# Kernel optimization log

Hardware: AMD Instinct MI355X
Metric: run time of the kernel (lower is better)

Reference implementation:

```python
import jax, jax.numpy as jnp
import numpy as np

# Sizes (match input_specs)
B = 50                 # number of CRN graphs in the batch
NS_PER, NR_PER = 2000, 4000
N_S, N_R = B * NS_PER, B * NR_PER   # 100k species, 200k reactions total
E = 1_000_000          # bipartite edges
D = 128                # d_model
L = 2                  # n_layers
N_TYPES, P_DIM = 16, 8
MAX_SPECIES_IDX = 2000


def setup_inputs() -> dict:
    key = jax.random.key(0)
    ks = jax.random.split(key, 12)
    inp = {
        "species_indices": jax.random.randint(ks[0], (N_S,), 0, MAX_SPECIES_IDX, dtype=jnp.int32),
        "is_external": jax.random.randint(ks[1], (N_S,), 0, 2, dtype=jnp.int32),
        "propensity_type_ids": jax.random.randint(ks[2], (N_R,), 0, N_TYPES, dtype=jnp.int32),
        "propensity_params": jax.random.normal(ks[3], (N_R, P_DIM), dtype=jnp.float32),
        "edge_species": jax.random.randint(ks[4], (E,), 0, N_S, dtype=jnp.int32),
        "edge_reaction": jax.random.randint(ks[5], (E,), 0, N_R, dtype=jnp.int32),
        # contiguous per-graph segment ids (graphs are equal-sized)
        "species_batch": jnp.repeat(jnp.arange(B, dtype=jnp.int32), NS_PER),
        "reaction_batch": jnp.repeat(jnp.arange(B, dtype=jnp.int32), NR_PER),
        # learned parameters
        "species_table": jax.random.normal(ks[6], (MAX_SPECIES_IDX, D), dtype=jnp.float32) * 0.02,
        "external_table": jax.random.normal(ks[7], (2, D), dtype=jnp.float32) * 0.02,
        "type_table": jax.random.normal(ks[8], (N_TYPES, D), dtype=jnp.float32) * 0.02,
        "W_param": jax.random.normal(ks[9], (P_DIM, D), dtype=jnp.float32) * 0.1,
        "b_param": jnp.zeros((D,), dtype=jnp.float32),
        # per-layer message-passing weights: concat([h, msg]) -> d
        "Wr": jax.random.normal(ks[10], (L, 2 * D, D), dtype=jnp.float32) * 0.05,
        "br": jnp.zeros((L, D), dtype=jnp.float32),
        "Ws": jax.random.normal(ks[11], (L, 2 * D, D), dtype=jnp.float32) * 0.05,
        "bs": jnp.zeros((L, D), dtype=jnp.float32),
    }
    return inp


def reference(species_indices, is_external, propensity_type_ids, propensity_params,
              edge_species, edge_reaction, species_batch, reaction_batch,
              species_table, external_table, type_table, W_param, b_param,
              Wr, br, Ws, bs):
    # Initial embeddings
    h_s = species_table[species_indices] + external_table[is_external]          # (N_S, D)
    h_r = type_table[propensity_type_ids] + propensity_params @ W_param + b_param  # (N_R, D)

    n_s, n_r = h_s.shape[0], h_r.shape[0]
    # Alternating bipartite sum message passing (SumMessagePassingLayer)
    for l in range(Wr.shape[0]):
        m_r = jax.ops.segment_sum(h_s[edge_species], edge_reaction, num_segments=n_r)
        h_r = jax.nn.relu(jnp.concatenate([h_r, m_r], axis=-1) @ Wr[l] + br[l])
        m_s = jax.ops.segment_sum(h_r[edge_reaction], edge_species, num_segments=n_s)
        h_s = jax.nn.relu(jnp.concatenate([h_s, m_s], axis=-1) @ Ws[l] + bs[l])

    # Segment-mean pooling per graph (index_add then divide by counts)
    pooled_s = jax.ops.segment_sum(h_s, species_batch, num_segments=B) / float(NS_PER)
    pooled_r = jax.ops.segment_sum(h_r, reaction_batch, num_segments=B) / float(NR_PER)
    context = jnp.concatenate([pooled_s, pooled_r], axis=-1)  # (B, 2D); dropout p=0 -> identity
    return context
```

## Files before the change

### kernel.cpp

```cpp
#include <hip/hip_runtime.h>
#include <stdint.h>

#define NS 100000
#define NR 200000
#define EE 1000000
#define DD 128
#define NB 50
#define NSP 2000
#define NRP 4000
#define BSH 10
#define NBR 196
#define NBS 98
#define CHUNK 8192

typedef short bf16x8 __attribute__((ext_vector_type(8)));
typedef float f32x4 __attribute__((ext_vector_type(4)));
typedef unsigned u32x4 __attribute__((ext_vector_type(4)));
typedef unsigned u32x2 __attribute__((ext_vector_type(2)));

__device__ __forceinline__ unsigned short f2bf(float f){
  unsigned u = __float_as_uint(f);
  u = (u + 0x7FFFu + ((u >> 16) & 1u)) >> 16;
  return (unsigned short)u;
}
__device__ __forceinline__ float bf2f(unsigned short s){
  return __uint_as_float(((unsigned)s) << 16);
}
__device__ __forceinline__ unsigned packbf(float a, float b){
  return (unsigned)f2bf(a) | ((unsigned)f2bf(b) << 16);
}
__device__ __forceinline__ float bflo(unsigned p){ return __uint_as_float(p << 16); }
__device__ __forceinline__ float bfhi(unsigned p){ return __uint_as_float(p & 0xFFFF0000u); }

__global__ void pack_w(const float* __restrict__ Wr, const float* __restrict__ Ws,
                       unsigned short* __restrict__ Wp){
  int g = blockIdx.x*256 + threadIdx.x;
  if (g >= 4*32768) return;
  int j = g & 7; int rest = g >> 3;
  int lane = rest & 63; rest >>= 6;
  int ks = rest & 7; rest >>= 3;
  int ct = rest & 7; int mat = rest >> 3;
  int k  = ks*32 + (lane >> 4)*8 + j;
  int cc = ct*16 + (lane & 15);
  const float* src = (mat < 2) ? (Wr + (size_t)mat*256*DD) : (Ws + (size_t)(mat-2)*256*DD);
  Wp[g] = f2bf(src[(size_t)k*DD + cc]);
}

__global__ __launch_bounds__(256) void init_all(const int* __restrict__ si, const int* __restrict__ ext,
        const int* __restrict__ tid, const float* __restrict__ pp,
        const float* __restrict__ st, const float* __restrict__ et, const float* __restrict__ tt,
        const float* __restrict__ Wpar, const float* __restrict__ bpar,
        unsigned short* __restrict__ hs, unsigned short* __restrict__ hr){
  int g = blockIdx.x*256 + threadIdx.x;
  int row = g >> 4, colb = (g & 15) * 8;
  if (row < NS){
    const float* a = st + (size_t)si[row]*DD + colb;
    const float* b = et + (size_t)ext[row]*DD + colb;
    float4 x0 = ((const float4*)a)[0], x1 = ((const float4*)a)[1];
    float4 y0 = ((const float4*)b)[0], y1 = ((const float4*)b)[1];
    u32x4 o;
    o.x = packbf(x0.x+y0.x, x0.y+y0.y);
    o.y = packbf(x0.z+y0.z, x0.w+y0.w);
    o.z = packbf(x1.x+y1.x, x1.y+y1.y);
    o.w = packbf(x1.z+y1.z, x1.w+y1.w);
    *(u32x4*)(hs + (size_t)row*DD + colb) = o;
  } else {
    int r = row - NS;
    const float* tb = tt + (size_t)tid[r]*DD + colb;
    float4 a0 = ((const float4*)tb)[0], a1 = ((const float4*)tb)[1];
    float4 b0 = ((const float4*)(bpar+colb))[0], b1 = ((const float4*)(bpar+colb))[1];
    a0.x += b0.x; a0.y += b0.y; a0.z += b0.z; a0.w += b0.w;
    a1.x += b1.x; a1.y += b1.y; a1.z += b1.z; a1.w += b1.w;
    const float* pr = pp + (size_t)r*8;
    float4 p0 = ((const float4*)pr)[0], p1 = ((const float4*)pr)[1];
    float w[8] = {p0.x,p0.y,p0.z,p0.w,p1.x,p1.y,p1.z,p1.w};
    #pragma unroll
    for (int p = 0; p < 8; p++){
      float4 w0 = ((const float4*)(Wpar + p*DD + colb))[0];
      float4 w1 = ((const float4*)(Wpar + p*DD + colb))[1];
      a0.x += w[p]*w0.x; a0.y += w[p]*w0.y; a0.z += w[p]*w0.z; a0.w += w[p]*w0.w;
      a1.x += w[p]*w1.x; a1.y += w[p]*w1.y; a1.z += w[p]*w1.z; a1.w += w[p]*w1.w;
    }
    u32x4 o;
    o.x = packbf(a0.x, a0.y); o.y = packbf(a0.z, a0.w);
    o.z = packbf(a1.x, a1.y); o.w = packbf(a1.z, a1.w);
    *(u32x4*)(hr + (size_t)r*DD + colb) = o;
  }
}

__global__ __launch_bounds__(256) void bucket_hist(const int* __restrict__ er, const int* __restrict__ es,
                                                   int* __restrict__ gcnt){
  __shared__ int cnt[NBR + NBS];
  int t = threadIdx.x;
  for (int j = t; j < NBR + NBS; j += 256) cnt[j] = 0;
  __syncthreads();
  long i0 = (long)blockIdx.x * 2048;
  for (int j = t; j < 2048; j += 256){
    long i = i0 + j;
    if (i < EE){
      atomicAdd(&cnt[er[i] >> BSH], 1);
      atomicAdd(&cnt[NBR + (es[i] >> BSH)], 1);
    }
  }
  __syncthreads();
  for (int j = t; j < NBR + NBS; j += 256)
    if (cnt[j]) atomicAdd(&gcnt[j], cnt[j]);
}

__global__ __launch_bounds__(256) void bucket_scan(const int* __restrict__ gcnt,
        int* __restrict__ bktOffR, int* __restrict__ bktOffS,
        int* __restrict__ gCurR, int* __restrict__ gCurS){
  __shared__ int a[256];
  int t = threadIdx.x;
  int own = (t < NBR) ? gcnt[t] : 0;
  a[t] = own; __syncthreads();
  for (int d = 1; d < 256; d <<= 1){
    int x = (t >= d) ? a[t-d] : 0;
    __syncthreads(); a[t] += x; __syncthreads();
  }
  if (t < NBR){ int v = a[t] - own; bktOffR[t] = v; gCurR[t] = v; }
  if (t == 0) bktOffR[NBR] = EE;
  __syncthreads();
  own = (t < NBS) ? gcnt[NBR + t] : 0;
  a[t] = own; __syncthreads();
  for (int d = 1; d < 256; d <<= 1){
    int x = (t >= d) ? a[t-d] : 0;
    __syncthreads(); a[t] += x; __syncthreads();
  }
  if (t < NBS){ int v = a[t] - own; bktOffS[t] = v; gCurS[t] = v; }
  if (t == 0) bktOffS[NBS] = EE;
}

__global__ __launch_bounds__(256) void bin_edges(const int* __restrict__ er, const int* __restrict__ es,
        int* __restrict__ gCurR, int* __restrict__ gCurS,
        unsigned* __restrict__ recR, unsigned* __restrict__ recS){
  __shared__ unsigned stage[CHUNK];
  __shared__ unsigned char stageb[CHUNK];
  __shared__ int cnt[256], scn[256], pref[256], gbase[256], lcur[256];
  int t = threadIdx.x;
  int side = blockIdx.y;
  const int* dest = side ? es : er;
  const int* srca = side ? er : es;
  int* gCur = side ? gCurS : gCurR;
  unsigned* rec = side ? recS : recR;
  int nbkt = side ? NBS : NBR;
  long i0 = (long)blockIdx.x * CHUNK;
  int n = (EE - i0 < CHUNK) ? (int)(EE - i0) : CHUNK;
  cnt[t] = 0;
  __syncthreads();
  for (int j = t; j < n; j += 256)
    atomicAdd(&cnt[dest[i0 + j] >> BSH], 1);
  __syncthreads();
  scn[t] = cnt[t];
  __syncthreads();
  for (int d = 1; d < 256; d <<= 1){
    int x = (t >= d) ? scn[t-d] : 0;
    __syncthreads(); scn[t] += x; __syncthreads();
  }
  pref[t] = scn[t] - cnt[t];
  lcur[t] = scn[t] - cnt[t];
  if (t < nbkt && cnt[t] > 0) gbase[t] = atomicAdd(&gCur[t], cnt[t]);
  __syncthreads();
  for (int j = t; j < n; j += 256){
    int d = dest[i0 + j];
    int s = srca[i0 + j];
    int b = d >> BSH;
    int p = atomicAdd(&lcur[b], 1);
    stage[p] = ((unsigned)(d - (b << BSH)) << 18) | (unsigned)s;
    stageb[p] = (unsigned char)b;
  }
  __syncthreads();
  for (int e = t; e < n; e += 256){
    int b = stageb[e];
    rec[gbase[b] + (e - pref[b])] = stage[e];
  }
}

__global__ __launch_bounds__(256) void build_csr(const unsigned* __restrict__ recR, const unsigned* __restrict__ recS,
        const int* __restrict__ bktOffR, const int* __restrict__ bktOffS,
        unsigned* __restrict__ csrR, unsigned* __restrict__ csrS,
        int* __restrict__ offsR, int* __restrict__ offsS){
  __shared__ int hist[1024], pref[1024], cur[1024], ws[256];
  int t = threadIdx.x;
  int bb = blockIdx.x;
  const unsigned* rec; const int* bktOff; unsigned* csr; int* offs; int N;
  if (bb < NBR){ rec = recR; bktOff = bktOffR; csr = csrR; offs = offsR; N = NR; }
  else { bb -= NBR; rec = recS; bktOff = bktOffS; csr = csrS; offs = offsS; N = NS; }
  int d0 = bb << BSH;
  int base = bktOff[bb], cnt_ = bktOff[bb+1] - base;
  #pragma unroll
  for (int j = 0; j < 4; j++) hist[t*4+j] = 0;
  __syncthreads();
  for (int e = t; e < cnt_; e += 256)
    atomicAdd(&hist[rec[base + e] >> 18], 1);
  __syncthreads();
  int s = 0, h[4];
  #pragma unroll
  for (int j = 0; j < 4; j++){ h[j] = hist[t*4+j]; s += h[j]; }
  ws[t] = s;
  __syncthreads();
  for (int d = 1; d < 256; d <<= 1){
    int x = (t >= d) ? ws[t-d] : 0;
    __syncthreads(); ws[t] += x; __syncthreads();
  }
  int run = ws[t] - s;
  #pragma unroll
  for (int j = 0; j < 4; j++){ pref[t*4+j] = run; cur[t*4+j] = base + run; run += h[j]; }
  __syncthreads();
  int DPB = N - d0; if (DPB > 1024) DPB = 1024;
  #pragma unroll
  for (int j = 0; j < 4; j++){
    int i = t*4 + j;
    if (i < DPB) offs[d0 + i] = base + pref[i];
  }
  if (t == 0 && d0 + DPB == N) offs[N] = EE;
  __syncthreads();
  for (int e = t; e < cnt_; e += 256){
    unsigned r = rec[base + e];
    int pos = atomicAdd(&cur[r >> 18], 1);
    csr[pos] = (((r >> 18) & 31u) << 26) | ((r & 0x3FFFFu) << 8);
  }
}

__global__ __launch_bounds__(256) void fused_layer(
        const unsigned short* __restrict__ gsrc,
        const unsigned short* __restrict__ hself,
        const int* __restrict__ offs, const unsigned* __restrict__ csr,
        const unsigned short* __restrict__ Wp, const float* __restrict__ bias,
        unsigned short* __restrict__ hout)
{
  __shared__ unsigned short msgT[32*DD];
  int t = threadIdx.x;
  int lane = t & 63;
  int w = t >> 6;
  int quad = lane >> 4, rlo = lane & 15;
  int row0 = blockIdx.x * 32;

  for (int i = t; i < 2048; i += 256) ((unsigned*)msgT)[i] = 0u;
  __syncthreads();

  {
    int rbeg = row0 + w*8;
    int k  = __builtin_amdgcn_readfirstlane(offs[rbeg]);
    int ke = __builtin_amdgcn_readfirstlane(offs[rbeg + 8]);
    int c16 = lane >> 2, sub4 = lane & 3;
    const char* gbase = (const char*)gsrc;
    float a0 = 0.f, a1 = 0.f;
    int cur = -1;
    unsigned rc[8]; unsigned pv[8];
    if (k < ke){
      #pragma unroll
      for (int i = 0; i < 8; i++){
        int kk = (k + i < ke) ? (k + i) : (ke - 1);
        rc[i] = (unsigned)__builtin_amdgcn_readfirstlane(csr[kk]);
      }
      #pragma unroll
      for (int i = 0; i < 8; i++)
        pv[i] = *(const unsigned*)(gbase + (rc[i] & 0x03FFFF00u) + lane*4);
      while (k < ke){
        unsigned rc2[8], pv2[8];
        int kn = k + 8;
        #pragma unroll
        for (int i = 0; i < 8; i++){
          int kk = (kn + i < ke) ? (kn + i) : (ke - 1);
          rc2[i] = (unsigned)__builtin_amdgcn_readfirstlane(csr[kk]);
        }
        #pragma unroll
        for (int i = 0; i < 8; i++)
          pv2[i] = *(const unsigned*)(gbase + (rc2[i] & 0x03FFFF00u) + lane*4);
        #pragma unroll
        for (int i = 0; i < 8; i++){
          if (k + i < ke){
            int dl = (int)(rc[i] >> 26);
            if (dl != cur){
              if (cur >= 0)
                *(unsigned*)(msgT + cur*DD + ((c16 ^ (cur & 7)) << 3) + (sub4 << 1)) = packbf(a0, a1);
              a0 = 0.f; a1 = 0.f;
              cur = dl;
            }
            a0 += bflo(pv[i]); a1 += bfhi(pv[i]);
          }
        }
        #pragma unroll
        for (int i = 0; i < 8; i++){ rc[i] = rc2[i]; pv[i] = pv2[i]; }
        k = kn;
      }
      if (cur >= 0)
        *(unsigned*)(msgT + cur*DD + ((c16 ^ (cur & 7)) << 3) + (sub4 << 1)) = packbf(a0, a1);
    }
  }
  __syncthreads();

  int ct0 = w * 2;
  bf16x8 wf[16];
  #pragma unroll
  for (int ks = 0; ks < 8; ks++){
    wf[ks*2+0] = *(const bf16x8*)(Wp + (size_t)(((ct0+0)*8 + ks)*64 + lane) * 8);
    wf[ks*2+1] = *(const bf16x8*)(Wp + (size_t)(((ct0+1)*8 + ks)*64 + lane) * 8);
  }
  bf16x8 Hb0[4], Hb1[4];
  #pragma unroll
  for (int ks = 0; ks < 4; ks++){
    int kloc = ks*32 + quad*8;
    Hb0[ks] = *(const bf16x8*)(hself + (size_t)(row0 + rlo) * DD + kloc);
    Hb1[ks] = *(const bf16x8*)(hself + (size_t)(row0 + 16 + rlo) * DD + kloc);
  }
  bf16x8 Mb0[4], Mb1[4];
  #pragma unroll
  for (int ks2 = 0; ks2 < 4; ks2++){
    int c8 = ks2*4 + quad;
    int lr0 = rlo, lr1 = 16 + rlo;
    Mb0[ks2] = *(const bf16x8*)(msgT + lr0*DD + ((c8 ^ (lr0 & 7)) * 8));
    Mb1[ks2] = *(const bf16x8*)(msgT + lr1*DD + ((c8 ^ (lr1 & 7)) * 8));
  }

  f32x4 acc[2][2];
  #pragma unroll
  for (int i = 0; i < 2; i++)
    #pragma unroll
    for (int j = 0; j < 2; j++){ f32x4 z = {0.f,0.f,0.f,0.f}; acc[i][j] = z; }

  #pragma unroll
  for (int ks = 0; ks < 4; ks++){
    acc[0][0] = __builtin_amdgcn_mfma_f32_16x16x32_bf16(wf[ks*2+0], Hb0[ks], acc[0][0], 0, 0, 0);
    acc[0][1] = __builtin_amdgcn_mfma_f32_16x16x32_bf16(wf[ks*2+1], Hb0[ks], acc[0][1], 0, 0, 0);
    acc[1][0] = __builtin_amdgcn_mfma_f32_16x16x32_bf16(wf[ks*2+0], Hb1[ks], acc[1][0], 0, 0, 0);
    acc[1][1] = __builtin_amdgcn_mfma_f32_16x16x32_bf16(wf[ks*2+1], Hb1[ks], acc[1][1], 0, 0, 0);
  }
  #pragma unroll
  for (int ks2 = 0; ks2 < 4; ks2++){
    int ks = 4 + ks2;
    acc[0][0] = __builtin_amdgcn_mfma_f32_16x16x32_bf16(wf[ks*2+0], Mb0[ks2], acc[0][0], 0, 0, 0);
    acc[0][1] = __builtin_amdgcn_mfma_f32_16x16x32_bf16(wf[ks*2+1], Mb0[ks2], acc[0][1], 0, 0, 0);
    acc[1][0] = __builtin_amdgcn_mfma_f32_16x16x32_bf16(wf[ks*2+0], Mb1[ks2], acc[1][0], 0, 0, 0);
    acc[1][1] = __builtin_amdgcn_mfma_f32_16x16x32_bf16(wf[ks*2+1], Mb1[ks2], acc[1][1], 0, 0, 0);
  }

  #pragma unroll
  for (int c = 0; c < 2; c++){
    float4 bv = *(const float4*)(bias + (ct0+c)*16 + quad*4);
    #pragma unroll
    for (int rb = 0; rb < 2; rb++){
      int row = row0 + rb*16 + rlo;
      float v0 = acc[rb][c][0] + bv.x;
      float v1 = acc[rb][c][1] + bv.y;
      float v2 = acc[rb][c][2] + bv.z;
      float v3 = acc[rb][c][3] + bv.w;
      v0 = v0 > 0.f ? v0 : 0.f;
      v1 = v1 > 0.f ? v1 : 0.f;
      v2 = v2 > 0.f ? v2 : 0.f;
      v3 = v3 > 0.f ? v3 : 0.f;
      u32x2 o; o.x = packbf(v0, v1); o.y = packbf(v2, v3);
      *(u32x2*)(hout + (size_t)row*DD + (ct0+c)*16 + quad*4) = o;
    }
  }
}

__global__ __launch_bounds__(256) void pool(const unsigned short* __restrict__ hs,
        const unsigned short* __restrict__ hr, float* __restrict__ out){
  __shared__ float red[16][128];
  int b = blockIdx.x, part = blockIdx.y;
  int t = threadIdx.x;
  int rg = t >> 4, sub = t & 15;
  const unsigned short* src; int row0, outoff; float scale;
  if (part < 4){ src = hs; row0 = b*NSP + part*500; outoff = b*256; scale = 1.f/NSP; }
  else { src = hr; row0 = b*NRP + (part-4)*500; outoff = b*256 + 128; scale = 1.f/NRP; }
  float a0=0,a1=0,a2=0,a3=0,a4=0,a5=0,a6=0,a7=0;
  for (int r = rg; r < 500; r += 16){
    u32x4 p = *(const u32x4*)(src + (size_t)(row0+r)*DD + sub*8);
    a0 += bflo(p.x); a1 += bfhi(p.x);
    a2 += bflo(p.y); a3 += bfhi(p.y);
    a4 += bflo(p.z); a5 += bfhi(p.z);
    a6 += bflo(p.w); a7 += bfhi(p.w);
  }
  float* rr = &red[rg][sub*8];
  rr[0]=a0; rr[1]=a1; rr[2]=a2; rr[3]=a3; rr[4]=a4; rr[5]=a5; rr[6]=a6; rr[7]=a7;
  __syncthreads();
  if (t < 128){
    float s = 0.f;
    #pragma unroll
    for (int g = 0; g < 16; g++) s += red[g][t];
    atomicAdd(&out[outoff + t], s * scale);
  }
}

extern "C" void kernel_launch(void* const* d_in, const int* in_sizes, int n_in,
                              void* d_out, int out_size, void* d_ws, size_t ws_size,
                              hipStream_t stream)
{
  const int*   si   = (const int*)d_in[0];
  const int*   ext  = (const int*)d_in[1];
  const int*   tid  = (const int*)d_in[2];
  const float* pp   = (const float*)d_in[3];
  const int*   es   = (const int*)d_in[4];
  const int*   er   = (const int*)d_in[5];
  const float* st   = (const float*)d_in[8];
  const float* et   = (const float*)d_in[9];
  const float* tt   = (const float*)d_in[10];
  const float* Wpar = (const float*)d_in[11];
  const float* bpar = (const float*)d_in[12];
  const float* Wr   = (const float*)d_in[13];
  const float* br   = (const float*)d_in[14];
  const float* Ws   = (const float*)d_in[15];
  const float* bs   = (const float*)d_in[16];
  float* out = (float*)d_out;

  char* basep = (char*)d_ws; size_t off = 0;
  auto alloc = [&](size_t bytes)->char*{
    char* r = basep + off; off = (off + bytes + 255) & ~(size_t)255; return r;
  };
  unsigned short* hs0 = (unsigned short*)alloc((size_t)NS*DD*2);
  unsigned short* hs1 = (unsigned short*)alloc((size_t)NS*DD*2);
  unsigned short* hr0 = (unsigned short*)alloc((size_t)NR*DD*2);
  unsigned short* hr1 = (unsigned short*)alloc((size_t)NR*DD*2);
  unsigned short* Wp  = (unsigned short*)alloc((size_t)4*32768*2);
  int* offsR = (int*)alloc((size_t)(NR+1)*4);
  int* offsS = (int*)alloc((size_t)(NS+1)*4);
  unsigned* csrR = (unsigned*)alloc((size_t)EE*4);
  unsigned* csrS = (unsigned*)alloc((size_t)EE*4);
  int* gcnt   = (int*)alloc(2048);
  int* bktOffR= (int*)alloc(2048);
  int* bktOffS= (int*)alloc(2048);
  int* gCurR  = (int*)alloc(2048);
  int* gCurS  = (int*)alloc(2048);
  unsigned* recR = (unsigned*)hs1;
  unsigned* recS = (unsigned*)hr1;

  hipMemsetAsync(gcnt, 0, 2048, stream);
  hipMemsetAsync(d_out, 0, (size_t)out_size*4, stream);

  pack_w<<<512, 256, 0, stream>>>(Wr, Ws, Wp);
  init_all<<<(NS+NR)*16/256, 256, 0, stream>>>(si, ext, tid, pp, st, et, tt, Wpar, bpar, hs0, hr0);

  bucket_hist<<<(EE + 2047)/2048, 256, 0, stream>>>(er, es, gcnt);
  bucket_scan<<<1, 256, 0, stream>>>(gcnt, bktOffR, bktOffS, gCurR, gCurS);
  bin_edges<<<dim3((EE + CHUNK - 1)/CHUNK, 2), 256, 0, stream>>>(er, es, gCurR, gCurS, recR, recS);
  build_csr<<<NBR + NBS, 256, 0, stream>>>(recR, recS, bktOffR, bktOffS, csrR, csrS, offsR, offsS);

  fused_layer<<<NR/32, 256, 0, stream>>>(hs0, hr0, offsR, csrR, Wp + (size_t)0*32768, br + (size_t)0*DD, hr1);
  fused_layer<<<NS/32, 256, 0, stream>>>(hr1, hs0, offsS, csrS, Wp + (size_t)2*32768, bs + (size_t)0*DD, hs1);
  fused_layer<<<NR/32, 256, 0, stream>>>(hs1, hr1, offsR, csrR, Wp + (size_t)1*32768, br + (size_t)1*DD, hr0);
  fused_layer<<<NS/32, 256, 0, stream>>>(hr0, hs1, offsS, csrS, Wp + (size_t)3*32768, bs + (size_t)1*DD, hs0);

  pool<<<dim3(NB, 12), 256, 0, stream>>>(hs0, hr0, out);
}
```

Before: 463.2 us.

## Stream gathered neighbor rows into LDS ring via async global_load_lds pipeline

Replaces the register double-buffered gather of source-node bf16 rows with a three-stage per-wave ring in LDS filled by global_load_lds, using explicit vmcnt waits so two batches of 8 edges stay in flight while one is reduced. It also drops the initial barrier after zeroing msgT by having each wave zero its own slice. The aim is deeper memory-level parallelism and less register pressure in the latency-bound edge gather. In exchange it uses more LDS per block, which may reduce occupancy, and the hand-written waitcnt/sched_barrier logic is fragile: if the compiler emits other vector memory ops inside the loop, the counts will be wrong.

```diff
diff --git a/kernel.cpp b/kernel.cpp
--- a/kernel.cpp
+++ b/kernel.cpp
@@ -12,6 +12,7 @@
 #define NBR 196
 #define NBS 98
 #define CHUNK 8192
+#define RING 24
 
 typedef short bf16x8 __attribute__((ext_vector_type(8)));
 typedef float f32x4 __attribute__((ext_vector_type(4)));
@@ -23,14 +24,15 @@
   u = (u + 0x7FFFu + ((u >> 16) & 1u)) >> 16;
   return (unsigned short)u;
 }
-__device__ __forceinline__ float bf2f(unsigned short s){
-  return __uint_as_float(((unsigned)s) << 16);
-}
 __device__ __forceinline__ unsigned packbf(float a, float b){
   return (unsigned)f2bf(a) | ((unsigned)f2bf(b) << 16);
 }
 __device__ __forceinline__ float bflo(unsigned p){ return __uint_as_float(p << 16); }
 __device__ __forceinline__ float bfhi(unsigned p){ return __uint_as_float(p & 0xFFFF0000u); }
+
+#define GLOAD_LDS4(gp, lp) __builtin_amdgcn_global_load_lds( \
+    (const __attribute__((address_space(1))) void*)(gp), \
+    (__attribute__((address_space(3))) void*)(lp), 4, 0, 0)
 
 __global__ void pack_w(const float* __restrict__ Wr, const float* __restrict__ Ws,
                        unsigned short* __restrict__ Wp){
@@ -230,66 +232,93 @@
         unsigned short* __restrict__ hout)
 {
   __shared__ unsigned short msgT[32*DD];
+  __shared__ unsigned ring[4*RING*64];
   int t = threadIdx.x;
   int lane = t & 63;
   int w = t >> 6;
   int quad = lane >> 4, rlo = lane & 15;
   int row0 = blockIdx.x * 32;
 
-  for (int i = t; i < 2048; i += 256) ((unsigned*)msgT)[i] = 0u;
-  __syncthreads();
+  {
+    u32x4 z4 = {0u,0u,0u,0u};
+    ((u32x4*)msgT)[w*128 + lane]      = z4;
+    ((u32x4*)msgT)[w*128 + 64 + lane] = z4;
+  }
 
   {
     int rbeg = row0 + w*8;
-    int k  = __builtin_amdgcn_readfirstlane(offs[rbeg]);
-    int ke = __builtin_amdgcn_readfirstlane(offs[rbeg + 8]);
+    int kp0 = __builtin_amdgcn_readfirstlane(offs[rbeg]);
+    int ke  = __builtin_amdgcn_readfirstlane(offs[rbeg + 8]);
     int c16 = lane >> 2, sub4 = lane & 3;
     const char* gbase = (const char*)gsrc;
+    unsigned* wring = ring + w*RING*64;
     float a0 = 0.f, a1 = 0.f;
     int cur = -1;
-    unsigned rc[8]; unsigned pv[8];
-    if (k < ke){
-      #pragma unroll
-      for (int i = 0; i < 8; i++){
-        int kk = (k + i < ke) ? (k + i) : (ke - 1);
-        rc[i] = (unsigned)__builtin_amdgcn_readfirstlane(csr[kk]);
-      }
-      #pragma unroll
-      for (int i = 0; i < 8; i++)
-        pv[i] = *(const unsigned*)(gbase + (rc[i] & 0x03FFFF00u) + lane*4);
-      while (k < ke){
-        unsigned rc2[8], pv2[8];
-        int kn = k + 8;
+    int nb = (ke - kp0 + 7) >> 3;
+
+    if (nb > 0){
+      unsigned recA[8], recB[8], recC[8];
+
+      auto fetchrec = [&](unsigned* R, int kb){
         #pragma unroll
         for (int i = 0; i < 8; i++){
-          int kk = (kn + i < ke) ? (kn + i) : (ke - 1);
-          rc2[i] = (unsigned)__builtin_amdgcn_readfirstlane(csr[kk]);
+          int kk = kb + i; if (kk > ke-1) kk = ke-1;
+          R[i] = (unsigned)__builtin_amdgcn_readfirstlane(csr[kk]);
         }
-        #pragma unroll
-        for (int i = 0; i < 8; i++)
-          pv2[i] = *(const unsigned*)(gbase + (rc2[i] & 0x03FFFF00u) + lane*4);
+      };
+      auto issue = [&](const unsigned* R, int bank){
         #pragma unroll
         for (int i = 0; i < 8; i++){
-          if (k + i < ke){
-            int dl = (int)(rc[i] >> 26);
+          const char* gp = gbase + (R[i] & 0x03FFFF00u) + (size_t)lane*4;
+          unsigned* lp = wring + (bank*8 + i)*64;
+          GLOAD_LDS4(gp, lp);
+        }
+      };
+      auto process = [&](const unsigned* R, int bank, int kb){
+        #pragma unroll
+        for (int i = 0; i < 8; i++){
+          if (kb + i < ke){
+            int dl = (int)(R[i] >> 26);
             if (dl != cur){
               if (cur >= 0)
                 *(unsigned*)(msgT + cur*DD + ((c16 ^ (cur & 7)) << 3) + (sub4 << 1)) = packbf(a0, a1);
               a0 = 0.f; a1 = 0.f;
               cur = dl;
             }
-            a0 += bflo(pv[i]); a1 += bfhi(pv[i]);
+            unsigned pv = wring[(bank*8 + i)*64 + lane];
+            a0 += bflo(pv); a1 += bfhi(pv);
           }
         }
-        #pragma unroll
-        for (int i = 0; i < 8; i++){ rc[i] = rc2[i]; pv[i] = pv2[i]; }
-        k = kn;
+      };
+
+      fetchrec(recA, kp0);                  issue(recA, 0);
+      if (nb > 1){ fetchrec(recB, kp0 + 8); issue(recB, 1); }
+      if (nb > 2){ fetchrec(recC, kp0 + 16); issue(recC, 2); }
+
+      int bank = 0;
+      for (int m = 0; m < nb; m++){
+        int r = nb - 1 - m;
+        if (r >= 2)      { asm volatile("s_waitcnt vmcnt(16)" ::: "memory"); }
+        else if (r == 1) { asm volatile("s_waitcnt vmcnt(8)"  ::: "memory"); }
+        else             { asm volatile("s_waitcnt vmcnt(0)"  ::: "memory"); }
+        __builtin_amdgcn_sched_barrier(0);
+
+        unsigned* R = (bank == 0) ? recA : (bank == 1) ? recB : recC;
+        process(R, bank, kp0 + m*8);
+        __builtin_amdgcn_sched_barrier(0);
+        if (m + 3 < nb){
+          fetchrec(R, kp0 + (m+3)*8);
+          issue(R, bank);
+        }
+        bank = (bank == 2) ? 0 : bank + 1;
       }
       if (cur >= 0)
         *(unsigned*)(msgT + cur*DD + ((c16 ^ (cur & 7)) << 3) + (sub4 << 1)) = packbf(a0, a1);
     }
   }
-  __syncthreads();
+  asm volatile("s_waitcnt vmcnt(0)" ::: "memory");
+  __syncthreads();
+  __builtin_amdgcn_sched_barrier(0);
 
   int ct0 = w * 2;
   bf16x8 wf[16];
```

Result: slower. 571.0 us (+23.3%).

## Gather two edges per wave with 8-byte loads and triple-buffered prefetch

Applied to the files above, without the earlier changes.

The CSR gather loop in the fused layer now splits each wave into two halves, each loading an 8-byte slice of a different neighbor row, so one wave load instruction covers two edges. The per-row reduction combines the halves with a cross-lane shuffle before writing to shared memory. Prefetch depth grows from double to triple buffering so more gather loads are in flight. Each wave zeroes its own shared-memory rows, which removes one block barrier. In exchange, the edge-pair merge logic adds branching and extra shuffles at every row boundary.

```diff
diff --git a/kernel.cpp b/kernel.cpp
--- a/kernel.cpp
+++ b/kernel.cpp
@@ -22,9 +22,6 @@
   unsigned u = __float_as_uint(f);
   u = (u + 0x7FFFu + ((u >> 16) & 1u)) >> 16;
   return (unsigned short)u;
-}
-__device__ __forceinline__ float bf2f(unsigned short s){
-  return __uint_as_float(((unsigned)s) << 16);
 }
 __device__ __forceinline__ unsigned packbf(float a, float b){
   return (unsigned)f2bf(a) | ((unsigned)f2bf(b) << 16);
@@ -236,57 +233,105 @@
   int quad = lane >> 4, rlo = lane & 15;
   int row0 = blockIdx.x * 32;
 
-  for (int i = t; i < 2048; i += 256) ((unsigned*)msgT)[i] = 0u;
-  __syncthreads();
+  {
+    u32x4 z4 = {0u,0u,0u,0u};
+    ((u32x4*)msgT)[w*128 + lane]      = z4;
+    ((u32x4*)msgT)[w*128 + 64 + lane] = z4;
+  }
 
   {
     int rbeg = row0 + w*8;
-    int k  = __builtin_amdgcn_readfirstlane(offs[rbeg]);
+    int kp = __builtin_amdgcn_readfirstlane(offs[rbeg]);
     int ke = __builtin_amdgcn_readfirstlane(offs[rbeg + 8]);
-    int c16 = lane >> 2, sub4 = lane & 3;
+    int half = lane >> 5;
+    int col4 = lane & 31;
     const char* gbase = (const char*)gsrc;
-    float a0 = 0.f, a1 = 0.f;
+    float a0 = 0.f, a1 = 0.f, a2 = 0.f, a3 = 0.f;
     int cur = -1;
-    unsigned rc[8]; unsigned pv[8];
-    if (k < ke){
-      #pragma unroll
-      for (int i = 0; i < 8; i++){
-        int kk = (k + i < ke) ? (k + i) : (ke - 1);
-        rc[i] = (unsigned)__builtin_amdgcn_readfirstlane(csr[kk]);
+
+    auto flushrow = [&](){
+      float s0 = a0 + __shfl_xor(a0, 32, 64);
+      float s1 = a1 + __shfl_xor(a1, 32, 64);
+      float s2 = a2 + __shfl_xor(a2, 32, 64);
+      float s3 = a3 + __shfl_xor(a3, 32, 64);
+      if (lane < 32){
+        u32x2 o; o.x = packbf(s0, s1); o.y = packbf(s2, s3);
+        *(u32x2*)(msgT + cur*DD + (((col4 >> 1) ^ (cur & 7)) * 8) + ((col4 & 1) * 4)) = o;
       }
-      #pragma unroll
-      for (int i = 0; i < 8; i++)
-        pv[i] = *(const unsigned*)(gbase + (rc[i] & 0x03FFFF00u) + lane*4);
-      while (k < ke){
-        unsigned rc2[8], pv2[8];
-        int kn = k + 8;
+      a0 = 0.f; a1 = 0.f; a2 = 0.f; a3 = 0.f;
+    };
+
+    if (kp < ke){
+      unsigned ra[8], rb[8], rcx[8];
+      u32x2 pa[4], pb[4], pc[4];
+
+      auto fetchrec = [&](unsigned* R, int kb){
         #pragma unroll
         for (int i = 0; i < 8; i++){
-          int kk = (kn + i < ke) ? (kn + i) : (ke - 1);
-          rc2[i] = (unsigned)__builtin_amdgcn_readfirstlane(csr[kk]);
+          int kk = kb + i; if (kk > ke-1) kk = ke-1;
+          R[i] = (unsigned)__builtin_amdgcn_readfirstlane(csr[kk]);
         }
+      };
+      auto issue = [&](const unsigned* R, u32x2* P){
         #pragma unroll
-        for (int i = 0; i < 8; i++)
-          pv2[i] = *(const unsigned*)(gbase + (rc2[i] & 0x03FFFF00u) + lane*4);
+        for (int j = 0; j < 4; j++){
+          unsigned rsel = half ? R[2*j+1] : R[2*j];
+          P[j] = *(const u32x2*)(gbase + (rsel & 0x03FFFF00u) + col4*8);
+        }
+      };
+      auto process = [&](const unsigned* R, const u32x2* P, int kb){
         #pragma unroll
-        for (int i = 0; i < 8; i++){
-          if (k + i < ke){
-            int dl = (int)(rc[i] >> 26);
-            if (dl != cur){
-              if (cur >= 0)
-                *(unsigned*)(msgT + cur*DD + ((c16 ^ (cur & 7)) << 3) + (sub4 << 1)) = packbf(a0, a1);
-              a0 = 0.f; a1 = 0.f;
-              cur = dl;
+        for (int j = 0; j < 4; j++){
+          if (kb + 2*j < ke){
+            int dl0 = (int)(R[2*j]   >> 26);
+            int dl1 = (int)(R[2*j+1] >> 26);
+            bool v1 = (kb + 2*j + 1 < ke);
+            u32x2 d = P[j];
+            if (dl0 != cur){ if (cur >= 0) flushrow(); cur = dl0; }
+            if (v1 && dl1 == dl0){
+              a0 += bflo(d.x); a1 += bfhi(d.x);
+              a2 += bflo(d.y); a3 += bfhi(d.y);
+            } else {
+              unsigned mU = half ? 0u : 0xFFFFFFFFu;
+              unsigned x = d.x & mU, y = d.y & mU;
+              a0 += bflo(x); a1 += bfhi(x);
+              a2 += bflo(y); a3 += bfhi(y);
+              if (v1){
+                flushrow(); cur = dl1;
+                unsigned mL = half ? 0xFFFFFFFFu : 0u;
+                x = d.x & mL; y = d.y & mL;
+                a0 += bflo(x); a1 += bfhi(x);
+                a2 += bflo(y); a3 += bfhi(y);
+              }
             }
-            a0 += bflo(pv[i]); a1 += bfhi(pv[i]);
           }
         }
-        #pragma unroll
-        for (int i = 0; i < 8; i++){ rc[i] = rc2[i]; pv[i] = pv2[i]; }
-        k = kn;
+      };
+
+      fetchrec(ra, kp); fetchrec(rb, kp + 8); fetchrec(rcx, kp + 16);
+      issue(ra, pa); issue(rb, pb);
+
+      int k = kp;
+      while (true){
+        if (k >= ke) break;
+        issue(rcx, pc);
+        process(ra, pa, k);
+        fetchrec(ra, k + 24);
+        k += 8;
+
+        if (k >= ke) break;
+        issue(ra, pa);
+        process(rb, pb, k);
+        fetchrec(rb, k + 24);
+        k += 8;
+
+        if (k >= ke) break;
+        issue(rb, pb);
+        process(rcx, pc, k);
+        fetchrec(rcx, k + 24);
+        k += 8;
       }
-      if (cur >= 0)
-        *(unsigned*)(msgT + cur*DD + ((c16 ^ (cur & 7)) << 3) + (sub4 << 1)) = packbf(a0, a1);
+      if (cur >= 0) flushrow();
     }
   }
   __syncthreads();
```

After: 477.4 us. 3.1% more time.

## Gather first-layer species messages from a compact 4000-row embedding table

Applied to the files above, without the earlier changes.

Layer 0's species-to-reaction aggregation now gathers from a small precomputed table of all (species_index, is_external) embedding combinations instead of the 100k-row species feature array. build_csr writes a second reaction CSR whose source field holds the combined table index, taken from a per-species index array that init_all emits. The aim is to make the first gather hit a 1 MB table that stays cache resident, replacing random reads over a 25 MB array. In exchange it adds a 4 MB CSR buffer, one more random read per edge during CSR build, and a small extra kernel.

```diff
diff --git a/kernel.cpp b/kernel.cpp
--- a/kernel.cpp
+++ b/kernel.cpp
@@ -22,9 +22,6 @@
   unsigned u = __float_as_uint(f);
   u = (u + 0x7FFFu + ((u >> 16) & 1u)) >> 16;
   return (unsigned short)u;
-}
-__device__ __forceinline__ float bf2f(unsigned short s){
-  return __uint_as_float(((unsigned)s) << 16);
 }
 __device__ __forceinline__ unsigned packbf(float a, float b){
   return (unsigned)f2bf(a) | ((unsigned)f2bf(b) << 16);
@@ -46,16 +43,37 @@
   Wp[g] = f2bf(src[(size_t)k*DD + cc]);
 }
 
+__global__ __launch_bounds__(256) void build_gtab(const float* __restrict__ st,
+        const float* __restrict__ et, unsigned short* __restrict__ gtab){
+  int g = blockIdx.x*256 + threadIdx.x;
+  if (g >= 4000*16) return;
+  int row = g >> 4, colb = (g & 15) * 8;
+  int i = row >> 1, e = row & 1;
+  const float* a = st + (size_t)i*DD + colb;
+  const float* b = et + (size_t)e*DD + colb;
+  float4 x0 = ((const float4*)a)[0], x1 = ((const float4*)a)[1];
+  float4 y0 = ((const float4*)b)[0], y1 = ((const float4*)b)[1];
+  u32x4 o;
+  o.x = packbf(x0.x+y0.x, x0.y+y0.y);
+  o.y = packbf(x0.z+y0.z, x0.w+y0.w);
+  o.z = packbf(x1.x+y1.x, x1.y+y1.y);
+  o.w = packbf(x1.z+y1.z, x1.w+y1.w);
+  *(u32x4*)(gtab + (size_t)row*DD + colb) = o;
+}
+
 __global__ __launch_bounds__(256) void init_all(const int* __restrict__ si, const int* __restrict__ ext,
         const int* __restrict__ tid, const float* __restrict__ pp,
         const float* __restrict__ st, const float* __restrict__ et, const float* __restrict__ tt,
         const float* __restrict__ Wpar, const float* __restrict__ bpar,
-        unsigned short* __restrict__ hs, unsigned short* __restrict__ hr){
+        unsigned short* __restrict__ hs, unsigned short* __restrict__ hr,
+        unsigned* __restrict__ didx){
   int g = blockIdx.x*256 + threadIdx.x;
   int row = g >> 4, colb = (g & 15) * 8;
   if (row < NS){
-    const float* a = st + (size_t)si[row]*DD + colb;
-    const float* b = et + (size_t)ext[row]*DD + colb;
+    int siv = si[row], exv = ext[row];
+    if ((g & 15) == 0) didx[row] = (unsigned)(((siv << 1) | exv) << 8);
+    const float* a = st + (size_t)siv*DD + colb;
+    const float* b = et + (size_t)exv*DD + colb;
     float4 x0 = ((const float4*)a)[0], x1 = ((const float4*)a)[1];
     float4 y0 = ((const float4*)b)[0], y1 = ((const float4*)b)[1];
     u32x4 o;
@@ -179,13 +197,14 @@
 __global__ __launch_bounds__(256) void build_csr(const unsigned* __restrict__ recR, const unsigned* __restrict__ recS,
         const int* __restrict__ bktOffR, const int* __restrict__ bktOffS,
         unsigned* __restrict__ csrR, unsigned* __restrict__ csrS,
-        int* __restrict__ offsR, int* __restrict__ offsS){
+        int* __restrict__ offsR, int* __restrict__ offsS,
+        const unsigned* __restrict__ didx, unsigned* __restrict__ csr0R){
   __shared__ int hist[1024], pref[1024], cur[1024], ws[256];
   int t = threadIdx.x;
   int bb = blockIdx.x;
-  const unsigned* rec; const int* bktOff; unsigned* csr; int* offs; int N;
-  if (bb < NBR){ rec = recR; bktOff = bktOffR; csr = csrR; offs = offsR; N = NR; }
-  else { bb -= NBR; rec = recS; bktOff = bktOffS; csr = csrS; offs = offsS; N = NS; }
+  const unsigned* rec; const int* bktOff; unsigned* csr; int* offs; int N; int isR;
+  if (bb < NBR){ rec = recR; bktOff = bktOffR; csr = csrR; offs = offsR; N = NR; isR = 1; }
+  else { bb -= NBR; rec = recS; bktOff = bktOffS; csr = csrS; offs = offsS; N = NS; isR = 0; }
   int d0 = bb << BSH;
   int base = bktOff[bb], cnt_ = bktOff[bb+1] - base;
   #pragma unroll
@@ -218,7 +237,9 @@
   for (int e = t; e < cnt_; e += 256){
     unsigned r = rec[base + e];
     int pos = atomicAdd(&cur[r >> 18], 1);
-    csr[pos] = (((r >> 18) & 31u) << 26) | ((r & 0x3FFFFu) << 8);
+    unsigned dl = ((r >> 18) & 31u) << 26;
+    csr[pos] = dl | ((r & 0x3FFFFu) << 8);
+    if (isR) csr0R[pos] = dl | didx[r & 0x3FFFFu];
   }
 }
 
@@ -416,8 +437,11 @@
   unsigned short* Wp  = (unsigned short*)alloc((size_t)4*32768*2);
   int* offsR = (int*)alloc((size_t)(NR+1)*4);
   int* offsS = (int*)alloc((size_t)(NS+1)*4);
-  unsigned* csrR = (unsigned*)alloc((size_t)EE*4);
-  unsigned* csrS = (unsigned*)alloc((size_t)EE*4);
+  unsigned* csrR  = (unsigned*)alloc((size_t)EE*4);
+  unsigned* csrS  = (unsigned*)alloc((size_t)EE*4);
+  unsigned* csr0R = (unsigned*)alloc((size_t)EE*4);
+  unsigned short* gtab = (unsigned short*)alloc((size_t)4000*DD*2);
+  unsigned* didx  = (unsigned*)alloc((size_t)NS*4);
   int* gcnt   = (int*)alloc(2048);
   int* bktOffR= (int*)alloc(2048);
   int* bktOffS= (int*)alloc(2048);
@@ -430,14 +454,15 @@
   hipMemsetAsync(d_out, 0, (size_t)out_size*4, stream);
 
   pack_w<<<512, 256, 0, stream>>>(Wr, Ws, Wp);
-  init_all<<<(NS+NR)*16/256, 256, 0, stream>>>(si, ext, tid, pp, st, et, tt, Wpar, bpar, hs0, hr0);
+  init_all<<<(NS+NR)*16/256, 256, 0, stream>>>(si, ext, tid, pp, st, et, tt, Wpar, bpar, hs0, hr0, didx);
+  build_gtab<<<(4000*16+255)/256, 256, 0, stream>>>(st, et, gtab);
 
   bucket_hist<<<(EE + 2047)/2048, 256, 0, stream>>>(er, es, gcnt);
   bucket_scan<<<1, 256, 0, stream>>>(gcnt, bktOffR, bktOffS, gCurR, gCurS);
   bin_edges<<<dim3((EE + CHUNK - 1)/CHUNK, 2), 256, 0, stream>>>(er, es, gCurR, gCurS, recR, recS);
-  build_csr<<<NBR + NBS, 256, 0, stream>>>(recR, recS, bktOffR, bktOffS, csrR, csrS, offsR, offsS);
-
-  fused_layer<<<NR/32, 256, 0, stream>>>(hs0, hr0, offsR, csrR, Wp + (size_t)0*32768, br + (size_t)0*DD, hr1);
+  build_csr<<<NBR + NBS, 256, 0, stream>>>(recR, recS, bktOffR, bktOffS, csrR, csrS, offsR, offsS, didx, csr0R);
+
+  fused_layer<<<NR/32, 256, 0, stream>>>(gtab, hr0, offsR, csr0R, Wp + (size_t)0*32768, br + (size_t)0*DD, hr1);
   fused_layer<<<NS/32, 256, 0, stream>>>(hr1, hs0, offsS, csrS, Wp + (size_t)2*32768, bs + (size_t)0*DD, hs1);
   fused_layer<<<NR/32, 256, 0, stream>>>(hs1, hr1, offsR, csrR, Wp + (size_t)1*32768, br + (size_t)1*DD, hr0);
   fused_layer<<<NS/32, 256, 0, stream>>>(hr0, hs1, offsS, csrS, Wp + (size_t)3*32768, bs + (size_t)1*DD, hs0);
```

Result: no change. 465.1 us (+0.4%).
